# Performance work log

Measured on AMD Instinct MI355X. Metric: run time of the kernel, lower is better.

The kernel has to match this reference:

```python
import jax, jax.numpy as jnp
import numpy as np
import math

B, S, D, H = 2, 2048, 64, 8

def setup_inputs() -> dict:
    key = jax.random.key(0)
    k1, k2, k3, k4 = jax.random.split(key, 4)
    return {
        "x1": jax.random.normal(k1, (B, S, D), dtype=jnp.float32),
        "x2": jax.random.normal(k2, (B, S, D), dtype=jnp.float32),
        "x3": jax.random.normal(k3, (B, H, S, S), dtype=jnp.float32),
        "x4": jax.random.normal(k4, (B, S, D), dtype=jnp.float32),
    }

def reference(x1, x2, x3, x4):
    d = x1.shape[-1]
    # qk: [B,S,S]
    qk = jnp.einsum('bsd,btd->bst', x1, x2) / jnp.sqrt(jnp.asarray(d, x1.dtype))
    # broadcast add bias -> [B,H,S,S]
    scores = qk[:, None, :, :] + x3
    attn = jax.nn.softmax(scores, axis=-1)
    # attn @ x4 with broadcast over H -> [B,H,S,D]
    out = jnp.einsum('bhst,btd->bhsd', attn, x4)
    return out
```

## Files before the change

### kernel.cpp

```cpp
#include <hip/hip_runtime.h>

#define B_ 2
#define S_ 2048
#define D_ 64
#define H_ 8

typedef __bf16 bf16x8 __attribute__((ext_vector_type(8)));
typedef float  f32x16 __attribute__((ext_vector_type(16)));
typedef float  f32x4  __attribute__((ext_vector_type(4)));
typedef unsigned int u32x4 __attribute__((ext_vector_type(4)));

#define C_QK 0.18033688011112042f
#define C_B  1.4426950408889634f

__device__ __forceinline__ unsigned int pkbf(float a, float b) {
    __bf16 x = (__bf16)a, y = (__bf16)b;
    unsigned short ux = __builtin_bit_cast(unsigned short, x);
    unsigned short uy = __builtin_bit_cast(unsigned short, y);
    return (unsigned int)ux | ((unsigned int)uy << 16);
}

__global__ __launch_bounds__(64, 1) void attn_kernel(
    const float* __restrict__ x1, const float* __restrict__ x2,
    const float* __restrict__ x3, const float* __restrict__ x4,
    float* __restrict__ out)
{
    const int lane = threadIdx.x;
    const int lo = lane & 31;
    const int hi = lane >> 5;

    const int bid = blockIdx.x;
    const int b   = bid >> 9;
    const int rem = bid & 511;
    const int h   = rem >> 6;
    const int qt  = rem & 63;
    const int qbase = qt * 32;

    const float* qrow = x1 + ((size_t)b * S_ + qbase + lo) * D_ + 8 * hi;
    bf16x8 Qf[4];
#pragma unroll
    for (int kk = 0; kk < 4; ++kk) {
        f32x4 qa = *(const f32x4*)(qrow + 16 * kk);
        f32x4 qb = *(const f32x4*)(qrow + 16 * kk + 4);
#pragma unroll
        for (int i = 0; i < 4; ++i) {
            Qf[kk][i]     = (__bf16)qa[i];
            Qf[kk][4 + i] = (__bf16)qb[i];
        }
    }

    f32x16 O0, O1;
#pragma unroll
    for (int i = 0; i < 16; ++i) { O0[i] = 0.f; O1[i] = 0.f; }
    float m_run = -3.0e38f;
    float l_run = 0.f;

    const float* brow = x3 + (((size_t)(b * H_ + h) * S_) + qbase + lo) * S_ + 4 * hi;

    auto load_bias = [&](int t, f32x4* dst) {
        const float* p = brow + t * 32;
#pragma unroll
        for (int g = 0; g < 4; ++g) dst[g] = *(const f32x4*)(p + 8 * g);
    };

    auto mk_pfrag = [&](const float* p) -> bf16x8 {
        int a0 = (int)pkbf(p[0], p[1]), a1 = (int)pkbf(p[2], p[3]);
        int b0 = (int)pkbf(p[4], p[5]), b1 = (int)pkbf(p[6], p[7]);
        int s0 = hi ? a0 : b0, s1 = hi ? a1 : b1;
        int r0 = __shfl_xor(s0, 32);
        int r1 = __shfl_xor(s1, 32);
        u32x4 f;
        f[0] = (unsigned int)(hi ? r0 : a0);
        f[1] = (unsigned int)(hi ? r1 : a1);
        f[2] = (unsigned int)(hi ? b0 : r0);
        f[3] = (unsigned int)(hi ? b1 : r1);
        return __builtin_bit_cast(bf16x8, f);
    };

    auto compute = [&](int t, const f32x4* bias) {
        const int tb = t * 32;

        const float* krow = x2 + ((size_t)b * S_ + tb + lo) * D_ + 8 * hi;
        f32x4 kraw[8];
#pragma unroll
        for (int kk = 0; kk < 4; ++kk) {
            kraw[2 * kk]     = *(const f32x4*)(krow + 16 * kk);
            kraw[2 * kk + 1] = *(const f32x4*)(krow + 16 * kk + 4);
        }
        float vraw[4][8];
#pragma unroll
        for (int g2 = 0; g2 < 2; ++g2) {
#pragma unroll
            for (int dh = 0; dh < 2; ++dh) {
                const float* vb = x4 + ((size_t)b * S_ + tb + 16 * g2 + 8 * hi) * D_ + 32 * dh + lo;
#pragma unroll
                for (int i = 0; i < 8; ++i) vraw[2 * g2 + dh][i] = vb[i * D_];
            }
        }

        f32x16 acc;
#pragma unroll
        for (int i = 0; i < 16; ++i) acc[i] = 0.f;
#pragma unroll
        for (int kk = 0; kk < 4; ++kk) {
            bf16x8 kf;
#pragma unroll
            for (int i = 0; i < 4; ++i) {
                kf[i]     = (__bf16)kraw[2 * kk][i];
                kf[4 + i] = (__bf16)kraw[2 * kk + 1][i];
            }
            acc = __builtin_amdgcn_mfma_f32_32x32x16_bf16(kf, Qf[kk], acc, 0, 0, 0);
        }

        float s[16];
#pragma unroll
        for (int r = 0; r < 16; ++r)
            s[r] = acc[r] * C_QK + bias[r >> 2][r & 3] * C_B;

        float pmax = s[0];
#pragma unroll
        for (int r = 1; r < 16; ++r) pmax = fmaxf(pmax, s[r]);
        pmax = fmaxf(pmax, __shfl_xor(pmax, 32));

        if (__any(pmax > m_run)) {
            float mnew = fmaxf(m_run, pmax);
            float sc = __builtin_amdgcn_exp2f(m_run - mnew);
#pragma unroll
            for (int r = 0; r < 16; ++r) { O0[r] *= sc; O1[r] *= sc; }
            l_run *= sc;
            m_run = mnew;
        }

        float p[16];
        float ls = 0.f;
#pragma unroll
        for (int r = 0; r < 16; ++r) {
            p[r] = __builtin_amdgcn_exp2f(s[r] - m_run);
            ls += p[r];
        }
        l_run += ls;

#pragma unroll
        for (int g2 = 0; g2 < 2; ++g2) {
            bf16x8 pf = mk_pfrag(p + 8 * g2);
#pragma unroll
            for (int dh = 0; dh < 2; ++dh) {
                bf16x8 vf;
#pragma unroll
                for (int i = 0; i < 8; ++i) vf[i] = (__bf16)vraw[2 * g2 + dh][i];
                if (dh == 0) O0 = __builtin_amdgcn_mfma_f32_32x32x16_bf16(vf, pf, O0, 0, 0, 0);
                else         O1 = __builtin_amdgcn_mfma_f32_32x32x16_bf16(vf, pf, O1, 0, 0, 0);
            }
        }
    };

    f32x4 bA[4], bB[4];
    load_bias(0, bA);
    for (int t = 0; t < 64; t += 2) {
        load_bias(t + 1, bB);
        compute(t, bA);
        if (t + 2 < 64) load_bias(t + 2, bA);
        compute(t + 1, bB);
    }

    float Lt = l_run + __shfl_xor(l_run, 32);
    float inv = 1.0f / Lt;

    float* orow = out + (((size_t)(b * H_ + h) * S_) + qbase + lo) * D_;
#pragma unroll
    for (int g = 0; g < 4; ++g) {
        f32x4 w0, w1;
#pragma unroll
        for (int j = 0; j < 4; ++j) {
            w0[j] = O0[4 * g + j] * inv;
            w1[j] = O1[4 * g + j] * inv;
        }
        *(f32x4*)(orow + 8 * g + 4 * hi)      = w0;
        *(f32x4*)(orow + 32 + 8 * g + 4 * hi) = w1;
    }
}

extern "C" void kernel_launch(void* const* d_in, const int* in_sizes, int n_in,
                              void* d_out, int out_size, void* d_ws, size_t ws_size,
                              hipStream_t stream) {
    const float* x1 = (const float*)d_in[0];
    const float* x2 = (const float*)d_in[1];
    const float* x3 = (const float*)d_in[2];
    const float* x4 = (const float*)d_in[3];
    float* o = (float*)d_out;
    hipLaunchKernelGGL(attn_kernel, dim3(B_ * H_ * (S_ / 32)), dim3(64), 0, stream,
                       x1, x2, x3, x4, o);
}
```

Measured before the change: 455.1 us.

## Split key range across four waves per block and merge softmax partials in LDS

```diff
diff --git a/kernel.cpp b/kernel.cpp
--- a/kernel.cpp
+++ b/kernel.cpp
@@ -4,6 +4,8 @@
 #define S_ 2048
 #define D_ 64
 #define H_ 8
+#define WAVES 4
+#define TPW 16
 
 typedef __bf16 bf16x8 __attribute__((ext_vector_type(8)));
 typedef float  f32x16 __attribute__((ext_vector_type(16)));
@@ -20,12 +22,18 @@
     return (unsigned int)ux | ((unsigned int)uy << 16);
 }
 
-__global__ __launch_bounds__(64, 1) void attn_kernel(
+__global__ __launch_bounds__(256, 4) void attn_kernel(
     const float* __restrict__ x1, const float* __restrict__ x2,
     const float* __restrict__ x3, const float* __restrict__ x4,
     float* __restrict__ out)
 {
-    const int lane = threadIdx.x;
+    __shared__ float sO[WAVES][D_][32];
+    __shared__ float sm[WAVES][32];
+    __shared__ float sl[WAVES][32];
+
+    const int tid  = threadIdx.x;
+    const int w    = tid >> 6;
+    const int lane = tid & 63;
     const int lo = lane & 31;
     const int hi = lane >> 5;
 
@@ -154,30 +162,53 @@
         }
     };
 
+    const int t0 = w * TPW;
     f32x4 bA[4], bB[4];
-    load_bias(0, bA);
-    for (int t = 0; t < 64; t += 2) {
+    load_bias(t0, bA);
+    for (int t = t0; t < t0 + TPW; t += 2) {
         load_bias(t + 1, bB);
         compute(t, bA);
-        if (t + 2 < 64) load_bias(t + 2, bA);
+        if (t + 2 < t0 + TPW) load_bias(t + 2, bA);
         compute(t + 1, bB);
     }
 
-    float Lt = l_run + __shfl_xor(l_run, 32);
-    float inv = 1.0f / Lt;
-
-    float* orow = out + (((size_t)(b * H_ + h) * S_) + qbase + lo) * D_;
+    float l_tot = l_run + __shfl_xor(l_run, 32);
+    if (hi == 0) { sm[w][lo] = m_run; sl[w][lo] = l_tot; }
+    __syncthreads();
+
+    float M = fmaxf(fmaxf(sm[0][lo], sm[1][lo]), fmaxf(sm[2][lo], sm[3][lo]));
+    float scale = __builtin_amdgcn_exp2f(m_run - M);
+    float Lsum = 0.f;
+#pragma unroll
+    for (int w2 = 0; w2 < WAVES; ++w2)
+        Lsum += sl[w2][lo] * __builtin_amdgcn_exp2f(sm[w2][lo] - M);
+
 #pragma unroll
     for (int g = 0; g < 4; ++g) {
-        f32x4 w0, w1;
 #pragma unroll
         for (int j = 0; j < 4; ++j) {
-            w0[j] = O0[4 * g + j] * inv;
-            w1[j] = O1[4 * g + j] * inv;
-        }
-        *(f32x4*)(orow + 8 * g + 4 * hi)      = w0;
-        *(f32x4*)(orow + 32 + 8 * g + 4 * hi) = w1;
-    }
+            int d = 8 * g + 4 * hi + j;
+            sO[w][d][lo]      = O0[4 * g + j] * scale;
+            sO[w][d + 32][lo] = O1[4 * g + j] * scale;
+        }
+    }
+    __syncthreads();
+
+    const float inv = 1.0f / Lsum;
+    const int d0 = (2 * w + hi) * 8;
+    f32x4 r0, r1;
+#pragma unroll
+    for (int i = 0; i < 4; ++i) {
+        float a = sO[0][d0 + i][lo] + sO[1][d0 + i][lo]
+                + sO[2][d0 + i][lo] + sO[3][d0 + i][lo];
+        float c = sO[0][d0 + 4 + i][lo] + sO[1][d0 + 4 + i][lo]
+                + sO[2][d0 + 4 + i][lo] + sO[3][d0 + 4 + i][lo];
+        r0[i] = a * inv;
+        r1[i] = c * inv;
+    }
+    float* orow = out + (((size_t)(b * H_ + h) * S_) + qbase + lo) * D_ + d0;
+    *(f32x4*)orow       = r0;
+    *(f32x4*)(orow + 4) = r1;
 }
 
 extern "C" void kernel_launch(void* const* d_in, const int* in_sizes, int n_in,
@@ -188,6 +219,6 @@
     const float* x3 = (const float*)d_in[2];
     const float* x4 = (const float*)d_in[3];
     float* o = (float*)d_out;
-    hipLaunchKernelGGL(attn_kernel, dim3(B_ * H_ * (S_ / 32)), dim3(64), 0, stream,
+    hipLaunchKernelGGL(attn_kernel, dim3(B_ * H_ * (S_ / 32)), dim3(256), 0, stream,
                        x1, x2, x3, x4, o);
 }
```

Result: slower. 590.1 us (+29.7%).
